# Kernel optimization log

Hardware: AMD Instinct MI355X
Metric: run time of the kernel (lower is better)

The kernel has to match this reference:

```python
import jax, jax.numpy as jnp
import numpy as np

HEADS = 48
HEAD_DIM = 64
DIM = 3072
RANK = 128
TEXT_LEN = 226
VID_LEN = 1822
B = 1
LORA_W = 1.0
EPS = 1e-5


def setup_inputs() -> dict:
    key = jax.random.key(0)
    ks = jax.random.split(key, 24)
    s = 0.02  # weight init scale
    inp = {
        "hidden_states": jax.random.normal(ks[0], (B, VID_LEN, DIM), jnp.float32),
        "encoder_hidden_states": jax.random.normal(ks[1], (B, TEXT_LEN, DIM), jnp.float32),
        "rope_cos": jax.random.uniform(ks[2], (VID_LEN, HEAD_DIM), jnp.float32),
        "rope_sin": jax.random.uniform(ks[3], (VID_LEN, HEAD_DIM), jnp.float32),
        "Wq": jax.random.normal(ks[4], (DIM, DIM), jnp.float32) * s,
        "bq": jax.random.normal(ks[5], (DIM,), jnp.float32) * s,
        "Wk": jax.random.normal(ks[6], (DIM, DIM), jnp.float32) * s,
        "bk": jax.random.normal(ks[7], (DIM,), jnp.float32) * s,
        "Wv": jax.random.normal(ks[8], (DIM, DIM), jnp.float32) * s,
        "bv": jax.random.normal(ks[9], (DIM,), jnp.float32) * s,
        "Wo": jax.random.normal(ks[10], (DIM, DIM), jnp.float32) * s,
        "bo": jax.random.normal(ks[11], (DIM,), jnp.float32) * s,
        "lq_down": jax.random.normal(ks[12], (RANK, DIM), jnp.float32) / RANK,
        "lq_up": jax.random.normal(ks[13], (DIM, RANK), jnp.float32) * s,
        "lk_down": jax.random.normal(ks[14], (RANK, DIM), jnp.float32) / RANK,
        "lk_up": jax.random.normal(ks[15], (DIM, RANK), jnp.float32) * s,
        "lv_down": jax.random.normal(ks[16], (RANK, DIM), jnp.float32) / RANK,
        "lv_up": jax.random.normal(ks[17], (DIM, RANK), jnp.float32) * s,
        "lp_down": jax.random.normal(ks[18], (RANK, DIM), jnp.float32) / RANK,
        "lp_up": jax.random.normal(ks[19], (DIM, RANK), jnp.float32) * s,
        "gamma_q": jnp.ones((HEAD_DIM,), jnp.float32),
        "beta_q": jnp.zeros((HEAD_DIM,), jnp.float32),
        "gamma_k": jnp.ones((HEAD_DIM,), jnp.float32),
        "beta_k": jnp.zeros((HEAD_DIM,), jnp.float32),
    }
    return inp


def _lora(x, down, up):
    # x: [B,S,DIM]; down: [RANK,DIM]; up: [DIM,RANK]
    return (x @ down.T) @ up.T


def _layernorm(x, gamma, beta):
    mu = jnp.mean(x, axis=-1, keepdims=True)
    var = jnp.mean(jnp.square(x - mu), axis=-1, keepdims=True)
    return (x - mu) * jax.lax.rsqrt(var + EPS) * gamma + beta


def _apply_rope(x, cos, sin):
    # diffusers apply_rotary_emb, use_real=True, unbind_dim=-1
    # x: [B,H,S,D]; cos/sin: [S,D]
    xr = x.reshape(*x.shape[:-1], HEAD_DIM // 2, 2)
    x1, x2 = xr[..., 0], xr[..., 1]
    x_rot = jnp.stack([-x2, x1], axis=-1).reshape(x.shape)
    return x * cos + x_rot * sin


def reference(hidden_states, encoder_hidden_states, rope_cos, rope_sin,
              Wq, bq, Wk, bk, Wv, bv, Wo, bo,
              lq_down, lq_up, lk_down, lk_up, lv_down, lv_up, lp_down, lp_up,
              gamma_q, beta_q, gamma_k, beta_k):
    h = jnp.concatenate([encoder_hidden_states, hidden_states], axis=1)  # [B,S,DIM]
    S = h.shape[1]

    q = h @ Wq.T + bq + _lora(h, lq_down, lq_up) * LORA_W
    k = h @ Wk.T + bk + _lora(h, lk_down, lk_up) * LORA_W
    v = h @ Wv.T + bv + _lora(h, lv_down, lv_up) * LORA_W

    def split_heads(x):  # [B,S,DIM] -> [B,H,S,D]
        return x.reshape(B, S, HEADS, HEAD_DIM).transpose(0, 2, 1, 3)

    q, k, v = split_heads(q), split_heads(k), split_heads(v)
    q = _layernorm(q, gamma_q, beta_q)
    k = _layernorm(k, gamma_k, beta_k)

    # RoPE on video tokens only
    q = q.at[:, :, TEXT_LEN:].set(_apply_rope(q[:, :, TEXT_LEN:], rope_cos, rope_sin))
    k = k.at[:, :, TEXT_LEN:].set(_apply_rope(k[:, :, TEXT_LEN:], rope_cos, rope_sin))

    # scaled dot-product attention (no mask, no dropout)
    scale = 1.0 / np.sqrt(HEAD_DIM).astype(np.float32)
    scores = jnp.einsum("bhqd,bhkd->bhqk", q, k) * scale
    probs = jax.nn.softmax(scores, axis=-1)
    attn_out = jnp.einsum("bhqk,bhkd->bhqd", probs, v)

    out = attn_out.transpose(0, 2, 1, 3).reshape(B, S, DIM)
    out = out @ Wo.T + bo + _lora(out, lp_down, lp_up) * LORA_W

    enc_out = out[:, :TEXT_LEN, :]
    hid_out = out[:, TEXT_LEN:, :]
    return (hid_out, enc_out)
```

## Files before the change

kernel.cpp:

```cpp
#include <hip/hip_runtime.h>
#include <hip/hip_bf16.h>
#include <stdint.h>

#define S_TOT 2048
#define TEXT 226
#define VID 1822
#define DIM 3072
#define NH 48
#define HD 64

typedef __bf16 bf16x8 __attribute__((ext_vector_type(8)));
typedef __bf16 bf16x4 __attribute__((ext_vector_type(4)));
typedef float f32x4 __attribute__((ext_vector_type(4)));

#define AS1 __attribute__((address_space(1)))
#define AS3 __attribute__((address_space(3)))

__device__ __forceinline__ void g2l16(const void* g, void* l) {
    __builtin_amdgcn_global_load_lds((const AS1 uint32_t*)(uintptr_t)g,
                                     (AS3 uint32_t*)(uintptr_t)l, 16, 0, 0);
}

__device__ __forceinline__ f32x4 mfma16(bf16x4 a, bf16x4 b, f32x4 c) {
#if __has_builtin(__builtin_amdgcn_mfma_f32_16x16x16bf16_1k)
    typedef short s4 __attribute__((ext_vector_type(4)));
    union U { bf16x4 b; s4 s; };
    U ua, ub; ua.b = a; ub.b = b;
    return __builtin_amdgcn_mfma_f32_16x16x16bf16_1k(ua.s, ub.s, c, 0, 0, 0);
#else
    f32x4 d = c;
    asm volatile("v_mfma_f32_16x16x16_bf16 %0, %1, %2, %0"
                 : "+v"(d) : "v"(a), "v"(b));
    return d;
#endif
}

#define ARENA_N 47431680ull

struct NormArgs { const void* p[24]; };

__global__ __launch_bounds__(256)
void normalize_inputs(NormArgs a, __bf16* __restrict__ arena)
{
    static constexpr unsigned long long segStart[25] = {
        0ull, 694272ull, 6291456ull, 15728640ull, 25165824ull, 34603008ull,
        44040192ull, 44433408ull, 44826624ull, 45219840ull, 45613056ull,
        46006272ull, 46399488ull, 46792704ull, 47185920ull, 47302528ull,
        47419136ull, 47422208ull, 47425280ull, 47428352ull, 47431424ull,
        47431488ull, 47431552ull, 47431616ull, 47431680ull };
    static constexpr int segIn[24] = {
        1, 0, 4, 6, 8, 10, 12, 13, 14, 15, 16, 17, 18, 19, 2, 3,
        5, 7, 9, 11, 20, 21, 22, 23 };

    const uint32_t w0 = *(const uint32_t*)a.p[20];
    const bool f32in = (w0 == 0x3F800000u);

    const size_t i0 = ((size_t)blockIdx.x * 256 + threadIdx.x) * 8;
    if (i0 >= ARENA_N) return;
    int s = 0;
    while (i0 >= segStart[s + 1]) s++;
    const size_t off = i0 - segStart[s];

    if (f32in) {
        const float* src = (const float*)a.p[segIn[s]] + off;
        const float4 v0 = ((const float4*)src)[0];
        const float4 v1 = ((const float4*)src)[1];
        bf16x8 o;
        o[0] = (__bf16)v0.x; o[1] = (__bf16)v0.y; o[2] = (__bf16)v0.z; o[3] = (__bf16)v0.w;
        o[4] = (__bf16)v1.x; o[5] = (__bf16)v1.y; o[6] = (__bf16)v1.z; o[7] = (__bf16)v1.w;
        *(bf16x8*)(arena + i0) = o;
    } else {
        const __bf16* src = (const __bf16*)a.p[segIn[s]] + off;
        *(uint4*)(arena + i0) = *(const uint4*)src;
    }
}

__device__ __forceinline__ void mm_chunks(
    const __bf16* __restrict__ Ag, int lda, const __bf16* __restrict__ Bg, int ldb,
    int kbeg, int kend, f32x4 (&acc)[4][4], __bf16* As, __bf16* Bs,
    int wave, int srow, int schk, int rdoff, int l15, int wm, int wn)
{
    for (int k0 = kbeg; k0 < kend; k0 += 32) {
        __syncthreads();
#pragma unroll
        for (int i = 0; i < 2; i++) {
            const int blk = i * 4 + wave;
            const int r = blk * 16 + srow;
            g2l16(Ag + (size_t)r * lda + k0 + schk, &As[blk * 512]);
            g2l16(Bg + (size_t)r * ldb + k0 + schk, &Bs[blk * 512]);
        }
        __syncthreads();
        bf16x8 af[4], bfr[4];
#pragma unroll
        for (int i = 0; i < 4; i++)
            af[i] = *(const bf16x8*)&As[(wm + i * 16 + l15) * 32 + rdoff];
#pragma unroll
        for (int j = 0; j < 4; j++)
            bfr[j] = *(const bf16x8*)&Bs[(wn + j * 16 + l15) * 32 + rdoff];
#pragma unroll
        for (int i = 0; i < 4; i++)
#pragma unroll
            for (int j = 0; j < 4; j++)
                acc[i][j] = __builtin_amdgcn_mfma_f32_16x16x32_bf16(af[i], bfr[j], acc[i][j], 0, 0, 0);
    }
}

template<int MODE>
__global__ __launch_bounds__(256)
void gemm_bt(const __bf16* __restrict__ A, int lda,
             const __bf16* __restrict__ B0, const __bf16* __restrict__ B1,
             const __bf16* __restrict__ B2, int ldb,
             const __bf16* __restrict__ bias0, const __bf16* __restrict__ bias1,
             const __bf16* __restrict__ bias2,
             __bf16* __restrict__ Cb, int ldc, int K, int tilesPerGroup,
             void* __restrict__ dout, const void* __restrict__ probe)
{
    __shared__ __bf16 As[128 * 32];
    __shared__ __bf16 Bs[128 * 32];
    const int tid  = threadIdx.x;
    const int wave = tid >> 6;
    const int lane = tid & 63;
    const int l15  = lane & 15, quad = lane >> 4;
    const int bm = blockIdx.x, bn = blockIdx.y;
    const int group = bn / tilesPerGroup;
    const int nt    = bn - group * tilesPerGroup;
    const __bf16* B    = (group == 0) ? B0 : ((group == 1) ? B1 : B2);
    const __bf16* bias = (group == 0) ? bias0 : ((group == 1) ? bias1 : bias2);

    const int srow  = lane >> 2;
    const int schk  = ((((lane & 3) - (lane >> 3)) & 3)) * 8;
    const int rdoff = ((quad + (l15 >> 1)) & 3) * 8;
    const __bf16* Ag = A + (size_t)(bm * 128) * lda;
    const __bf16* Bg = B + (size_t)(nt * 128) * ldb;

    f32x4 acc[4][4] = {};
    const int wm = (wave & 1) * 64;
    const int wn = (wave >> 1) * 64;

    mm_chunks(Ag, lda, Bg, ldb, 0, K, acc, As, Bs, wave, srow, schk, rdoff, l15, wm, wn);

    bool f32out = false;
    if (MODE == 1) f32out = (*(const uint32_t*)probe == 0x3F800000u);

#pragma unroll
    for (int i = 0; i < 4; i++) {
#pragma unroll
        for (int j = 0; j < 4; j++) {
            const int coll = wn + j * 16 + l15;
            const int col  = bn * 128 + coll;
            float bv = 0.f;
            if (bias) bv = (float)bias[nt * 128 + coll];
#pragma unroll
            for (int r = 0; r < 4; r++) {
                const int row = bm * 128 + wm + i * 16 + quad * 4 + r;
                float v = acc[i][j][r] + bv;
                if (MODE == 1) {
                    const size_t mrow = (row < TEXT) ? (size_t)(row + VID) : (size_t)(row - TEXT);
                    if (f32out) ((float*)dout)[mrow * DIM + col] = v;
                    else        ((__bf16*)dout)[mrow * DIM + col] = (__bf16)v;
                } else {
                    Cb[(size_t)row * ldc + col] = (__bf16)v;
                }
            }
        }
    }
}

struct TpArgs { const __bf16* S[4]; __bf16* D[4]; };

__global__ __launch_bounds__(256)
void transp_ld(TpArgs a)
{
    __shared__ float tile[64][65];
    const __bf16* src = a.S[blockIdx.z];
    __bf16* dst = a.D[blockIdx.z];
    const int j0 = blockIdx.x * 64;
    const int r0 = blockIdx.y * 64;
    const int tid = threadIdx.x;
    const int rr = tid >> 4;
    const int cc = (tid & 15) * 4;
#pragma unroll
    for (int p = 0; p < 4; p++) {
        const int r = p * 16 + rr;
        const uint2 raw = *(const uint2*)&src[(size_t)(r0 + r) * DIM + j0 + cc];
        const __bf16* b = (const __bf16*)&raw;
#pragma unroll
        for (int e = 0; e < 4; e++) tile[r][cc + e] = (float)b[e];
    }
    __syncthreads();
#pragma unroll
    for (int p = 0; p < 4; p++) {
        const int j = p * 16 + rr;
        __bf16 o[4];
#pragma unroll
        for (int e = 0; e < 4; e++) o[e] = (__bf16)tile[cc + e][j];
        *(uint2*)&dst[(size_t)(j0 + j) * 128 + r0 + cc] = *(const uint2*)o;
    }
}

struct FoldArgs { const __bf16* A[4]; const __bf16* B[4]; const __bf16* W[4]; __bf16* D[4]; };

__global__ __launch_bounds__(256)
void fold_w(FoldArgs a)
{
    __shared__ __bf16 As[128 * 32];
    __shared__ __bf16 Bs[128 * 32];
    const int z = blockIdx.z;
    const int tid  = threadIdx.x;
    const int wave = tid >> 6;
    const int lane = tid & 63;
    const int l15  = lane & 15, quad = lane >> 4;
    const int bm = blockIdx.x, bn = blockIdx.y;

    const int srow  = lane >> 2;
    const int schk  = ((((lane & 3) - (lane >> 3)) & 3)) * 8;
    const int rdoff = ((quad + (l15 >> 1)) & 3) * 8;
    const __bf16* Ag = a.A[z] + (size_t)(bm * 128) * 128;
    const __bf16* Bg = a.B[z] + (size_t)(bn * 128) * 128;
    const __bf16* W  = a.W[z];
    __bf16* D = a.D[z];

    f32x4 acc[4][4] = {};
    const int wm = (wave & 1) * 64;
    const int wn = (wave >> 1) * 64;

    mm_chunks(Ag, 128, Bg, 128, 0, 128, acc, As, Bs, wave, srow, schk, rdoff, l15, wm, wn);

#pragma unroll
    for (int i = 0; i < 4; i++) {
#pragma unroll
        for (int j = 0; j < 4; j++) {
            const int col = bn * 128 + wn + j * 16 + l15;
#pragma unroll
            for (int r = 0; r < 4; r++) {
                const int row = bm * 128 + wm + i * 16 + quad * 4 + r;
                const size_t idx = (size_t)row * DIM + col;
                D[idx] = (__bf16)(acc[i][j][r] + (float)W[idx]);
            }
        }
    }
}

__global__ __launch_bounds__(256)
void ln_vt(const __bf16* __restrict__ qkv,
           const __bf16* __restrict__ gq, const __bf16* __restrict__ bq,
           const __bf16* __restrict__ gk, const __bf16* __restrict__ bk,
           const __bf16* __restrict__ cosb, const __bf16* __restrict__ sinb,
           __bf16* __restrict__ qh, __bf16* __restrict__ kh,
           __bf16* __restrict__ vt)
{
    __shared__ float tile[64][65];
    if (blockIdx.x < 2048) {
        const int s = blockIdx.x;
        const int wave = threadIdx.x >> 6, lane = threadIdx.x & 63;
        for (int idx = wave; idx < 2 * NH; idx += 4) {
            const int mat  = idx / NH;
            const int head = idx - mat * NH;
            float x = (float)qkv[(size_t)s * 9216 + mat * DIM + head * HD + lane];
            float mu = x;
            mu += __shfl_xor(mu, 1, 64);  mu += __shfl_xor(mu, 2, 64);
            mu += __shfl_xor(mu, 4, 64);  mu += __shfl_xor(mu, 8, 64);
            mu += __shfl_xor(mu, 16, 64); mu += __shfl_xor(mu, 32, 64);
            mu *= 0.015625f;
            float d = x - mu;
            float vv = d * d;
            vv += __shfl_xor(vv, 1, 64);  vv += __shfl_xor(vv, 2, 64);
            vv += __shfl_xor(vv, 4, 64);  vv += __shfl_xor(vv, 8, 64);
            vv += __shfl_xor(vv, 16, 64); vv += __shfl_xor(vv, 32, 64);
            vv *= 0.015625f;
            const float g = (float)(mat ? gk[lane] : gq[lane]);
            const float b = (float)(mat ? bk[lane] : bq[lane]);
            float y = d * rsqrtf(vv + 1e-5f) * g + b;
            if (s >= TEXT) {
                const int pos = s - TEXT;
                const float c  = (float)cosb[pos * HD + lane];
                const float sn = (float)sinb[pos * HD + lane];
                const float oth = __shfl_xor(y, 1, 64);
                const float rot = (lane & 1) ? oth : -oth;
                y = y * c + rot * sn;
            }
            if (mat == 0) y *= 0.125f;
            __bf16* dst = mat ? kh : qh;
            dst[((size_t)head * S_TOT + s) * HD + lane] = (__bf16)y;
        }
    } else {
        const int vb = blockIdx.x - 2048;
        const int h = vb >> 5, sb = vb & 31;
        const int tid = threadIdx.x;
        const int r0 = tid >> 4;
        const int c0 = (tid & 15) * 4;
#pragma unroll
        for (int p = 0; p < 4; p++) {
            const int r = p * 16 + r0;
            const uint2 raw = *(const uint2*)&qkv[((size_t)(sb * 64 + r)) * 9216 + 2 * DIM + h * HD + c0];
            const __bf16* b = (const __bf16*)&raw;
#pragma unroll
            for (int e = 0; e < 4; e++) tile[r][c0 + e] = (float)b[e];
        }
        __syncthreads();
#pragma unroll
        for (int p = 0; p < 4; p++) {
            const int d = p * 16 + r0;
            __bf16 o[4];
#pragma unroll
            for (int e = 0; e < 4; e++) o[e] = (__bf16)tile[c0 + e][d];
            *(uint2*)&vt[((size_t)(h * HD + d)) * S_TOT + sb * 64 + c0] = *(const uint2*)o;
        }
    }
}

#define KS_LD 72
#define VS_LD 136
#define NKB (S_TOT / 128)

__device__ __forceinline__ void fa_load(const __bf16* __restrict__ kh,
                                        const __bf16* __restrict__ vt,
                                        int h, int kb, int tid,
                                        bf16x8 (&kr)[4], bf16x8 (&vr)[4])
{
#pragma unroll
    for (int p = 0; p < 4; p++) {
        const int id = p * 256 + tid;
        const int krow = id >> 3, kc = (id & 7) * 8;
        kr[p] = *(const bf16x8*)(kh + ((size_t)(h * S_TOT + kb * 128 + krow)) * HD + kc);
        const int vrow = id >> 4, vc = (id & 15) * 8;
        vr[p] = *(const bf16x8*)(vt + ((size_t)(h * HD + vrow)) * S_TOT + kb * 128 + vc);
    }
}

__global__ __launch_bounds__(256)
void flash_attn(const __bf16* __restrict__ qh, const __bf16* __restrict__ kh,
                const __bf16* __restrict__ vt, __bf16* __restrict__ outp)
{
    __shared__ __bf16 Ks[128 * KS_LD];
    __shared__ __bf16 Vs[64 * VS_LD];
    const int qb = blockIdx.x, h = blockIdx.y;
    const int tid = threadIdx.x, wave = tid >> 6, lane = tid & 63;
    const int l15 = lane & 15, quad = lane >> 4;

    const __bf16* qp = qh + ((size_t)(h * S_TOT + qb * 64 + wave * 16 + l15)) * HD + quad * 8;
    const bf16x8 qf0 = *(const bf16x8*)qp;
    const bf16x8 qf1 = *(const bf16x8*)(qp + 32);

    f32x4 of[4] = {};
    float m_i = -1e30f, l_i = 0.f;
    const float L2E = 1.44269504f;

    bf16x8 kr[4], vr[4];
    fa_load(kh, vt, h, 0, tid, kr, vr);

    for (int kb = 0; kb < NKB; kb++) {
        __syncthreads();
#pragma unroll
        for (int p = 0; p < 4; p++) {
            const int id = p * 256 + tid;
            const int krow = id >> 3, kc = (id & 7) * 8;
            *(bf16x8*)&Ks[krow * KS_LD + kc] = kr[p];
            const int vrow = id >> 4, vc = (id & 15) * 8;
            *(bf16x8*)&Vs[vrow * VS_LD + vc] = vr[p];
        }
        __syncthreads();
        if (kb + 1 < NKB) fa_load(kh, vt, h, kb + 1, tid, kr, vr);

        f32x4 sf[8];
#pragma unroll
        for (int n = 0; n < 8; n++) {
            const bf16x8 k0 = *(const bf16x8*)&Ks[(n * 16 + l15) * KS_LD + quad * 8];
            const bf16x8 k1 = *(const bf16x8*)&Ks[(n * 16 + l15) * KS_LD + 32 + quad * 8];
            f32x4 z = {0.f, 0.f, 0.f, 0.f};
            z = __builtin_amdgcn_mfma_f32_16x16x32_bf16(k0, qf0, z, 0, 0, 0);
            sf[n] = __builtin_amdgcn_mfma_f32_16x16x32_bf16(k1, qf1, z, 0, 0, 0);
        }

        float mx = sf[0][0];
#pragma unroll
        for (int n = 0; n < 8; n++)
#pragma unroll
            for (int r = 0; r < 4; r++) mx = fmaxf(mx, sf[n][r]);
        mx = fmaxf(mx, __shfl_xor(mx, 16, 64));
        mx = fmaxf(mx, __shfl_xor(mx, 32, 64));
        const float mnew = fmaxf(m_i, mx);
        const float alpha = __builtin_amdgcn_exp2f((m_i - mnew) * L2E);
        m_i = mnew;
        float rs = 0.f;
#pragma unroll
        for (int n = 0; n < 8; n++)
#pragma unroll
            for (int r = 0; r < 4; r++) {
                const float pv = __builtin_amdgcn_exp2f((sf[n][r] - mnew) * L2E);
                sf[n][r] = pv;
                rs += pv;
            }
        rs += __shfl_xor(rs, 16, 64);
        rs += __shfl_xor(rs, 32, 64);
        l_i = l_i * alpha + rs;

        bf16x4 pf[8];
#pragma unroll
        for (int kk = 0; kk < 8; kk++) {
            bf16x4 o;
            o[0] = (__bf16)sf[kk][0]; o[1] = (__bf16)sf[kk][1];
            o[2] = (__bf16)sf[kk][2]; o[3] = (__bf16)sf[kk][3];
            pf[kk] = o;
        }

#pragma unroll
        for (int r = 0; r < 4; r++) {
            const float a_r = __shfl(alpha, quad * 4 + r, 16);
#pragma unroll
            for (int j = 0; j < 4; j++) of[j][r] *= a_r;
        }

#pragma unroll
        for (int kk = 0; kk < 8; kk++) {
#pragma unroll
            for (int j = 0; j < 4; j++) {
                const bf16x4 vf = *(const bf16x4*)&Vs[(j * 16 + l15) * VS_LD + kk * 16 + quad * 4];
                of[j] = mfma16(pf[kk], vf, of[j]);
            }
        }
    }

#pragma unroll
    for (int r = 0; r < 4; r++) {
        const float lr = __shfl(l_i, quad * 4 + r, 16);
        const float inv = 1.f / lr;
        const int row = qb * 64 + wave * 16 + quad * 4 + r;
#pragma unroll
        for (int j = 0; j < 4; j++)
            outp[(size_t)row * DIM + h * HD + j * 16 + l15] = (__bf16)(of[j][r] * inv);
    }
}

extern "C" void kernel_launch(void* const* d_in, const int* in_sizes, int n_in,
                              void* d_out, int out_size, void* d_ws, size_t ws_size,
                              hipStream_t stream)
{
    char* ws = (char*)d_ws;
    __bf16* arena = (__bf16*)ws;

    const __bf16* h     = arena + 0;
    const __bf16* Wq    = arena + 6291456;
    const __bf16* Wk    = arena + 15728640;
    const __bf16* Wv    = arena + 25165824;
    const __bf16* Wo    = arena + 34603008;
    const __bf16* lqd   = arena + 44040192;
    const __bf16* lqu   = arena + 44433408;
    const __bf16* lkd   = arena + 44826624;
    const __bf16* lku   = arena + 45219840;
    const __bf16* lvd   = arena + 45613056;
    const __bf16* lvu   = arena + 46006272;
    const __bf16* lpd   = arena + 46399488;
    const __bf16* lpu   = arena + 46792704;
    const __bf16* ropec = arena + 47185920;
    const __bf16* ropes = arena + 47302528;
    const __bf16* bq    = arena + 47419136;
    const __bf16* bk    = arena + 47422208;
    const __bf16* bv    = arena + 47425280;
    const __bf16* bo    = arena + 47428352;
    const __bf16* gq    = arena + 47431424;
    const __bf16* btq   = arena + 47431488;
    const __bf16* gk    = arena + 47431552;
    const __bf16* btk   = arena + 47431616;

    __bf16* ldT  = (__bf16*)(ws + 94863360);
    __bf16* qkvb = (__bf16*)(ws + 98009088);
    __bf16* Wpo  = (__bf16*)(ws + 135757824);
    __bf16* Wpq  = (__bf16*)(ws + 154632192);
    __bf16* Wpk  = (__bf16*)(ws + 173506560);
    __bf16* Wpv  = (__bf16*)(ws + 192380928);
    __bf16* qh   = (__bf16*)(ws + 154632192);
    __bf16* kh   = (__bf16*)(ws + 179798016);
    __bf16* vt   = (__bf16*)(ws + 12582912);
    __bf16* attn = (__bf16*)(ws + 0);

    NormArgs na;
    for (int i = 0; i < 24; i++) na.p[i] = d_in[i];
    normalize_inputs<<<(unsigned)((ARENA_N / 8 + 255) / 256), 256, 0, stream>>>(na, arena);

    TpArgs tp;
    tp.S[0] = lqd; tp.S[1] = lkd; tp.S[2] = lvd; tp.S[3] = lpd;
    tp.D[0] = ldT; tp.D[1] = ldT + 393216; tp.D[2] = ldT + 786432; tp.D[3] = ldT + 1179648;
    transp_ld<<<dim3(48, 2, 4), 256, 0, stream>>>(tp);

    FoldArgs fa;
    fa.A[0] = lqu; fa.A[1] = lku; fa.A[2] = lvu; fa.A[3] = lpu;
    fa.B[0] = tp.D[0]; fa.B[1] = tp.D[1]; fa.B[2] = tp.D[2]; fa.B[3] = tp.D[3];
    fa.W[0] = Wq; fa.W[1] = Wk; fa.W[2] = Wv; fa.W[3] = Wo;
    fa.D[0] = Wpq; fa.D[1] = Wpk; fa.D[2] = Wpv; fa.D[3] = Wpo;
    fold_w<<<dim3(24, 24, 4), 256, 0, stream>>>(fa);

    gemm_bt<3><<<dim3(16, 72), 256, 0, stream>>>(
        h, DIM, Wpq, Wpk, Wpv, DIM, bq, bk, bv,
        qkvb, 9216, DIM, 24, nullptr, nullptr);

    ln_vt<<<2048 + 1536, 256, 0, stream>>>(qkvb, gq, btq, gk, btk, ropec, ropes, qh, kh, vt);

    flash_attn<<<dim3(32, 48), 256, 0, stream>>>(qh, kh, vt, attn);

    gemm_bt<1><<<dim3(16, 24), 256, 0, stream>>>(
        attn, DIM, Wpo, Wpo, Wpo, DIM, bo, bo, bo,
        nullptr, DIM, DIM, 24, d_out, d_in[20]);
}
```

Measured before the change: 718.9 us.

## Replace QKV GEMM with 256x256-tile 8-wave kernel using pipelined async LDS loads

Replaces the 128x128-tile QKV projection GEMM with a dedicated kernel that uses 256x256 output tiles, 512 threads, and a double-buffered LDS pipeline fed by direct global-to-LDS loads. Loads for later k-steps are interleaved into the MFMA phases, with explicit vmcnt waits and raised wave priority during the math. A block-index swizzle is added for L2 locality. The goal is more data reuse per byte loaded and better overlap of memory with compute. In exchange, it uses 128KB of LDS and a large accumulator set, which limits occupancy to one block per CU, and the tile count is hardcoded for this shape.

```diff
diff --git a/kernel.cpp b/kernel.cpp
--- a/kernel.cpp
+++ b/kernel.cpp
@@ -162,6 +162,141 @@
                     Cb[(size_t)row * ldc + col] = (__bf16)v;
                 }
             }
+        }
+    }
+}
+
+#define QKV_NT 48
+#define QKV_NI 24
+
+__device__ __forceinline__ void barx() {
+    asm volatile("" ::: "memory");
+    __builtin_amdgcn_s_barrier();
+    asm volatile("" ::: "memory");
+}
+__device__ __forceinline__ void vmw6() { asm volatile("s_waitcnt vmcnt(6)" ::: "memory"); }
+__device__ __forceinline__ void vmw0() { asm volatile("s_waitcnt vmcnt(0)" ::: "memory"); }
+
+__device__ __forceinline__ void stage2(const __bf16* gsrc, __bf16* lds, size_t koff) {
+    g2l16(gsrc + koff,      lds);
+    g2l16(gsrc + koff + 32, lds + 8192);
+}
+
+__global__ __launch_bounds__(512)
+void gemm256_qkv(const __bf16* __restrict__ A,
+                 const __bf16* __restrict__ B0, const __bf16* __restrict__ B1,
+                 const __bf16* __restrict__ B2,
+                 const __bf16* __restrict__ bias0, const __bf16* __restrict__ bias1,
+                 const __bf16* __restrict__ bias2,
+                 __bf16* __restrict__ C)
+{
+    __shared__ __bf16 L[65536];
+
+    const int bid = blockIdx.x;
+    const int swz = (bid & 7) * 36 + (bid >> 3);
+    const int bm = swz % 8;
+    const int bn = swz / 8;
+    const int group = bn / 12;
+    const int nt    = bn - group * 12;
+    const __bf16* Bm   = (group == 0) ? B0 : ((group == 1) ? B1 : B2);
+    const __bf16* bias = (group == 0) ? bias0 : ((group == 1) ? bias1 : bias2);
+
+    const int tid = threadIdx.x, wave = tid >> 6, lane = tid & 63;
+    const int wr = wave >> 2, wc = wave & 3;
+    const int l15 = lane & 15, quad = lane >> 4;
+    const int srow  = lane >> 2;
+    const int schk  = ((((lane & 3) - (lane >> 3)) & 3)) * 8;
+    const int rdoff = ((quad + (l15 >> 1)) & 3) * 8;
+    const int rdbase = l15 * 32 + rdoff;
+
+    static constexpr int AL0[8] = {0,1,2,3, 8,9,10,11};
+    static constexpr int AL1[8] = {4,5,6,7, 12,13,14,15};
+    static constexpr int BL0[8] = {0,1,4,5, 8,9,12,13};
+    static constexpr int BL1[8] = {2,3,6,7, 10,11,14,15};
+    const int a0 = AL0[wave], a1 = AL1[wave], b0 = BL0[wave], b1 = BL1[wave];
+
+    const __bf16* Ag = A  + (size_t)(bm * 256) * DIM;
+    const __bf16* Bg = Bm + (size_t)(nt * 256) * DIM;
+    const __bf16* gA0 = Ag + (size_t)(a0 * 16 + srow) * DIM + schk;
+    const __bf16* gA1 = Ag + (size_t)(a1 * 16 + srow) * DIM + schk;
+    const __bf16* gB0 = Bg + (size_t)(b0 * 16 + srow) * DIM + schk;
+    const __bf16* gB1 = Bg + (size_t)(b1 * 16 + srow) * DIM + schk;
+
+#define STG_A0(BUF, T) stage2(gA0, &L[(BUF)*32768 +         a0*512], (size_t)(T)*64)
+#define STG_A1(BUF, T) stage2(gA1, &L[(BUF)*32768 +         a1*512], (size_t)(T)*64)
+#define STG_B0(BUF, T) stage2(gB0, &L[(BUF)*32768 + 16384 + b0*512], (size_t)(T)*64)
+#define STG_B1(BUF, T) stage2(gB1, &L[(BUF)*32768 + 16384 + b1*512], (size_t)(T)*64)
+
+    f32x4 acc[8][4] = {};
+
+    STG_A0(0, 0); STG_B0(0, 0); STG_A1(0, 0); STG_B1(0, 0);
+    STG_A0(1, 1); STG_B0(1, 1); STG_A1(1, 1);
+    vmw6();
+    barx();
+
+#define PH(BUF, MH, NH, STAGE, WAIT) do {                                        \
+    bf16x8 af[4][2], bfr[2][2];                                                  \
+    _Pragma("unroll")                                                            \
+    for (int mm = 0; mm < 4; mm++) {                                             \
+        af[mm][0] = *(const bf16x8*)&L[(BUF)*32768 +        (wr*8 + (MH)*4 + mm)*512 + rdbase]; \
+        af[mm][1] = *(const bf16x8*)&L[(BUF)*32768 + 8192 + (wr*8 + (MH)*4 + mm)*512 + rdbase]; \
+    }                                                                            \
+    _Pragma("unroll")                                                            \
+    for (int nn = 0; nn < 2; nn++) {                                             \
+        bfr[nn][0] = *(const bf16x8*)&L[(BUF)*32768 + 16384 +        (wc*4 + (NH)*2 + nn)*512 + rdbase]; \
+        bfr[nn][1] = *(const bf16x8*)&L[(BUF)*32768 + 16384 + 8192 + (wc*4 + (NH)*2 + nn)*512 + rdbase]; \
+    }                                                                            \
+    barx();                                                                      \
+    STAGE;                                                                       \
+    __builtin_amdgcn_s_setprio(1);                                               \
+    _Pragma("unroll")                                                            \
+    for (int mm = 0; mm < 4; mm++)                                               \
+        _Pragma("unroll")                                                        \
+        for (int nn = 0; nn < 2; nn++) {                                         \
+            acc[(MH)*4+mm][(NH)*2+nn] = __builtin_amdgcn_mfma_f32_16x16x32_bf16( \
+                af[mm][0], bfr[nn][0], acc[(MH)*4+mm][(NH)*2+nn], 0, 0, 0);      \
+            acc[(MH)*4+mm][(NH)*2+nn] = __builtin_amdgcn_mfma_f32_16x16x32_bf16( \
+                af[mm][1], bfr[nn][1], acc[(MH)*4+mm][(NH)*2+nn], 0, 0, 0);      \
+        }                                                                        \
+    __builtin_amdgcn_s_setprio(0);                                               \
+    WAIT;                                                                        \
+    barx();                                                                      \
+} while (0)
+
+#pragma unroll 1
+    for (int i = 0; i < QKV_NI; i++) {
+        const int t1 = 2 * i + 1, t2 = 2 * i + 2, t3 = 2 * i + 3;
+        const bool more = (i < QKV_NI - 1);
+        PH(0, 0, 0, { STG_B1(1, t1); },              { });
+        PH(0, 0, 1, { if (more) STG_A0(0, t2); },    { });
+        PH(0, 1, 0, { if (more) STG_B0(0, t2); },    { });
+        PH(0, 1, 1, { if (more) STG_A1(0, t2); },    { if (more) vmw6(); else vmw0(); });
+        PH(1, 0, 0, { if (more) STG_B1(0, t2); },    { });
+        PH(1, 0, 1, { if (more) STG_A0(1, t3); },    { });
+        PH(1, 1, 0, { if (more) STG_B0(1, t3); },    { });
+        PH(1, 1, 1, { if (more) STG_A1(1, t3); },    { if (more) vmw6(); else vmw0(); });
+    }
+#undef PH
+#undef STG_A0
+#undef STG_A1
+#undef STG_B0
+#undef STG_B1
+
+#pragma unroll
+    for (int mh = 0; mh < 2; mh++)
+#pragma unroll
+    for (int nh = 0; nh < 2; nh++)
+#pragma unroll
+    for (int nn = 0; nn < 2; nn++) {
+        const int coll = wc * 64 + nh * 32 + nn * 16 + l15;
+        const float bv = (float)bias[nt * 256 + coll];
+        const int col = bn * 256 + coll;
+#pragma unroll
+        for (int mm = 0; mm < 4; mm++) {
+            const int rowb = bm * 256 + wr * 128 + mh * 64 + mm * 16 + quad * 4;
+#pragma unroll
+            for (int r = 0; r < 4; r++)
+                C[(size_t)(rowb + r) * 9216 + col] = (__bf16)(acc[mh*4+mm][nh*2+nn][r] + bv);
         }
     }
 }
@@ -490,9 +625,7 @@
     fa.D[0] = Wpq; fa.D[1] = Wpk; fa.D[2] = Wpv; fa.D[3] = Wpo;
     fold_w<<<dim3(24, 24, 4), 256, 0, stream>>>(fa);
 
-    gemm_bt<3><<<dim3(16, 72), 256, 0, stream>>>(
-        h, DIM, Wpq, Wpk, Wpv, DIM, bq, bk, bv,
-        qkvb, 9216, DIM, 24, nullptr, nullptr);
+    gemm256_qkv<<<288, 512, 0, stream>>>(h, Wpq, Wpk, Wpv, bq, bk, bv, qkvb);
 
     ln_vt<<<2048 + 1536, 256, 0, stream>>>(qkvb, gq, btq, gk, btk, ropec, ropes, qh, kh, vt);
 
```

Measured after the change: 726.9 us. Within noise of the previous version (+1.1%).
